# Kernel tuning notes

Hardware: AMD Instinct MI355X
Metric: run time of the kernel (lower is better)

The kernel has to match this reference:

```python
import jax, jax.numpy as jnp
import numpy as np

DIM = 512
DIM_TIME = 64
DIM_FF = 2048
B, L = 2, 512
EPS = 1e-5


def _layer_norm(x, g, b):
    mu = jnp.mean(x, axis=-1, keepdims=True)
    var = jnp.mean((x - mu) ** 2, axis=-1, keepdims=True)
    return (x - mu) * jax.lax.rsqrt(var + EPS) * g + b


def _sioconv(u, wa, hid_re, hid_im):
    # u: (B, L, Dt) float. Faithful to the FFT/triu construction, expressed as
    # cumulative log-sums (linear conv with all-ones == causal cumsum).
    Bb, Ll, Dt = u.shape
    out = (u @ wa.T).reshape(Bb, Ll, Dt, 2)          # linear_a, view_as_complex
    a_sqr = out[..., 0] ** 2 + out[..., 1] ** 2
    a = (out[..., 0] + 1j * out[..., 1]) * (jax.lax.rsqrt(a_sqr) * jnp.exp(-a_sqr))
    a = jnp.transpose(a, (0, 2, 1))                  # (B, Dt, L)
    a_ln = jnp.log(a)
    S = jnp.cumsum(a_ln, axis=-1)                    # S_k = sum_{j<=k} ln a_j
    S_prev = jnp.concatenate([jnp.zeros_like(S[..., :1]), S[..., :-1]], axis=-1)
    # c[b,d,i,k] = exp(S_k - S_{i-1}) = prod_{j=i..k} a_j, kept for k >= i-1
    diff = S[:, :, None, :] - S_prev[:, :, :, None]  # (B, Dt, L, L)
    idx = jnp.arange(Ll)
    mask = idx[None, :] >= (idx[:, None] - 1)        # k >= i-1 (triu diag=-1)
    c = jnp.where(mask, jnp.exp(diff), 0.0)
    uc = jnp.transpose(u.astype(jnp.complex64), (0, 2, 1))   # (B, Dt, L)
    hidden = (hid_re + 1j * hid_im)[None, :] * jnp.ones((Bb, 1), jnp.complex64)
    xin = jnp.concatenate([hidden[..., None], uc[..., :-1]], axis=-1)  # rolled + h0
    h = jnp.einsum('bdik,bdk->bdi', c, xin)
    h = h.at[:, :, -1].add(uc[:, :, -1])
    return jnp.transpose(h.real, (0, 2, 1)).astype(u.dtype)


def _ffn(x, w1, b1, w2, b2):
    return jax.nn.silu(x @ w1.T + b1) @ w2.T + b2


def setup_inputs() -> dict:
    key = jax.random.key(0)
    ks = jax.random.split(key, 12)
    d, dt, dff = DIM, DIM_TIME, DIM_FF
    return {
        'x': jax.random.normal(ks[0], (B, L, d), jnp.float32),
        'ln1_g': jnp.ones((d,), jnp.float32), 'ln1_b': jnp.zeros((d,), jnp.float32),
        'fc_w': jax.random.normal(ks[1], (dt, d), jnp.float32) * d ** -0.5,
        'fc_b': jnp.zeros((dt,), jnp.float32),
        'lin_in_w': jax.random.normal(ks[2], (dt, d), jnp.float32) * d ** -0.5,
        'lin_in_b': jnp.zeros((dt,), jnp.float32),
        'wa': jax.random.normal(ks[3], (2 * dt, dt), jnp.float32) * dt ** -0.5,
        'hid_re': jax.random.normal(ks[4], (dt,), jnp.float32),
        'hid_im': jax.random.normal(ks[5], (dt,), jnp.float32),
        'lin_out_w': jax.random.normal(ks[6], (d, dt), jnp.float32) * dt ** -0.5,
        'lin_out_b': jnp.zeros((d,), jnp.float32),
        'ln2_g': jnp.ones((d,), jnp.float32), 'ln2_b': jnp.zeros((d,), jnp.float32),
        'w1': jax.random.normal(ks[7], (dff, d), jnp.float32) * d ** -0.5,
        'b1': jnp.zeros((dff,), jnp.float32),
        'w2': jax.random.normal(ks[8], (d, dff), jnp.float32) * dff ** -0.5,
        'b2': jnp.zeros((d,), jnp.float32),
    }


def reference(x, ln1_g, ln1_b, fc_w, fc_b, lin_in_w, lin_in_b, wa, hid_re, hid_im,
              lin_out_w, lin_out_b, ln2_g, ln2_b, w1, b1, w2, b2):
    x_res = x
    xn = _layer_norm(x, ln1_g, ln1_b)
    y = jax.nn.silu(xn @ fc_w.T + fc_b)                  # gate, (B, L, Dt)
    u = xn @ lin_in_w.T + lin_in_b                       # (B, L, Dt)
    h = _sioconv(u, wa, hid_re, hid_im)
    x = (h * y) @ lin_out_w.T + lin_out_b + x_res        # dropout = identity (eval)
    x_res = x
    x = _ffn(_layer_norm(x, ln2_g, ln2_b), w1, b1, w2, b2) + x_res
    return x
```

## Files before the change

### kernel.cpp

```cpp
#include <hip/hip_runtime.h>
#include <math.h>

#define LSEQ 512
#define DMODEL 512
#define DT 64
#define DFF 2048

typedef unsigned short u16;
typedef __attribute__((ext_vector_type(8))) short short8;
typedef __attribute__((ext_vector_type(4))) float f32x4;
typedef __attribute__((ext_vector_type(16))) float f32x16;

__device__ __forceinline__ float wave_sum(float v) {
#pragma unroll
  for (int o = 32; o > 0; o >>= 1) v += __shfl_xor(v, o, 64);
  return v;
}

__device__ __forceinline__ u16 f2bf(float f) {
  unsigned int u = __float_as_uint(f);
  u += 0x7fffu + ((u >> 16) & 1u);
  return (u16)(u >> 16);
}
__device__ __forceinline__ float bf2f(u16 h) {
  return __uint_as_float(((unsigned int)h) << 16);
}
__device__ __forceinline__ void splitbf(float f, u16& h, u16& l) {
  h = f2bf(f);
  l = f2bf(f - bf2f(h));
}
__device__ __forceinline__ void split8(const float* __restrict__ p,
                                       short8& bh, short8& bl) {
  float4 a = *(const float4*)p;
  float4 b = *(const float4*)(p + 4);
  float vv[8] = {a.x, a.y, a.z, a.w, b.x, b.y, b.z, b.w};
#pragma unroll
  for (int e = 0; e < 8; ++e) {
    u16 h, l; splitbf(vv[e], h, l);
    bh[e] = (short)h; bl[e] = (short)l;
  }
}


__global__ __launch_bounds__(512) void k_fa(
    const float* __restrict__ x, const float* __restrict__ g1,
    const float* __restrict__ be1,
    const float* __restrict__ fcw, const float* __restrict__ liw,
    const float* __restrict__ wa,
    const float* __restrict__ fcb, const float* __restrict__ lib,
    const float* __restrict__ w1, const float* __restrict__ w2,
    float* __restrict__ y_o, float* __restrict__ u_o,
    float* __restrict__ ar_o, float* __restrict__ ai_o,
    u16* __restrict__ w1s, u16* __restrict__ w2s)
{
  const int blk = blockIdx.x;
  if (blk >= 64) {
    for (int i = (blk - 64) * 512 + threadIdx.x; i < 524288; i += 131072) {
      if (i < 262144) {
        int r = i >> 7, c0 = (i & 127) << 2;
        float4 v = ((const float4*)w1)[i];
        ushort4 o;
        o.x = f2bf(v.x); o.y = f2bf(v.y); o.z = f2bf(v.z); o.w = f2bf(v.w);
        int lane_s = (r & 31) + (((c0 & 15) >> 3) << 5);
        int flat = (r >> 5) * 16384 + (c0 >> 4) * 512 + lane_s * 8 + (c0 & 7);
        *(ushort4*)(w1s + flat) = o;
      } else {
        int ii = i - 262144;
        int r = ii >> 9, c0 = (ii & 511) << 2;
        float4 v = ((const float4*)w2)[ii];
        ushort4 o;
        o.x = f2bf(v.x); o.y = f2bf(v.y); o.z = f2bf(v.z); o.w = f2bf(v.w);
        int lane_s = (r & 31) + (((c0 & 15) >> 3) << 5);
        int flat = (r >> 5) * 65536 + (c0 >> 4) * 512 + lane_s * 8 + (c0 & 7);
        *(ushort4*)(w2s + flat) = o;
      }
    }
    return;
  }
  __shared__ __align__(16) u16 xsh[16][520];
  __shared__ __align__(16) u16 xsl[16][520];
  __shared__ __align__(16) u16 ush[16][80];
  __shared__ __align__(16) u16 usl[16][80];
  const int tid = threadIdx.x;
  const int wv = tid >> 6, lane = tid & 63;
  const int lr = lane & 15, lk = lane >> 4;
  const int mt = blk;

#pragma unroll
  for (int rr = 0; rr < 2; ++rr) {
    const int r = wv * 2 + rr;
    const int row = mt * 16 + r;
    const float* xr = x + (size_t)row * DMODEL;
    float v[8]; float s = 0.f;
#pragma unroll
    for (int j = 0; j < 8; ++j) { v[j] = xr[lane + 64 * j]; s += v[j]; }
    s = wave_sum(s);
    const float mu = s * (1.f / 512.f);
    float q = 0.f;
#pragma unroll
    for (int j = 0; j < 8; ++j) { float dd = v[j] - mu; q += dd * dd; }
    q = wave_sum(q);
    const float rstd = rsqrtf(q * (1.f / 512.f) + 1e-5f);
#pragma unroll
    for (int j = 0; j < 8; ++j) {
      int idx = lane + 64 * j;
      float o = (v[j] - mu) * rstd * g1[idx] + be1[idx];
      u16 h, l; splitbf(o, h, l);
      xsh[r][idx] = h;
      xsl[r][idx] = l;
    }
  }
  __syncthreads();

  const int c = wv * 16 + lr;
  {
    const float* brow = (c < DT) ? (fcw + (size_t)c * DMODEL)
                                 : (liw + (size_t)(c - DT) * DMODEL);
    f32x4 acc = {};
#pragma unroll 4
    for (int k = 0; k < DMODEL; k += 32) {
      short8 ah = *(const short8*)&xsh[lr][k + lk * 8];
      short8 al = *(const short8*)&xsl[lr][k + lk * 8];
      short8 bh, bl;
      split8(brow + k + lk * 8, bh, bl);
      acc = __builtin_amdgcn_mfma_f32_16x16x32_bf16(ah, bh, acc, 0, 0, 0);
      acc = __builtin_amdgcn_mfma_f32_16x16x32_bf16(ah, bl, acc, 0, 0, 0);
      acc = __builtin_amdgcn_mfma_f32_16x16x32_bf16(al, bh, acc, 0, 0, 0);
    }
#pragma unroll
    for (int j = 0; j < 4; ++j) {
      int rl = lk * 4 + j;
      int row = mt * 16 + rl;
      float v = acc[j];
      if (c < DT) {
        v += fcb[c];
        y_o[row * DT + c] = v / (1.f + expf(-v));
      } else {
        int d = c - DT;
        v += lib[d];
        u_o[row * DT + d] = v;
        u16 h, l; splitbf(v, h, l);
        ush[rl][d] = h; usl[rl][d] = l;
      }
    }
  }
  __syncthreads();
  {
    const float* warow = wa + (size_t)c * DT;
    f32x4 acc = {};
#pragma unroll
    for (int ks = 0; ks < 2; ++ks) {
      short8 ah = *(const short8*)&ush[lr][ks * 32 + lk * 8];
      short8 al = *(const short8*)&usl[lr][ks * 32 + lk * 8];
      short8 bh, bl;
      split8(warow + ks * 32 + lk * 8, bh, bl);
      acc = __builtin_amdgcn_mfma_f32_16x16x32_bf16(ah, bh, acc, 0, 0, 0);
      acc = __builtin_amdgcn_mfma_f32_16x16x32_bf16(ah, bl, acc, 0, 0, 0);
      acc = __builtin_amdgcn_mfma_f32_16x16x32_bf16(al, bh, acc, 0, 0, 0);
    }
#pragma unroll
    for (int j = 0; j < 4; ++j) {
      float v = acc[j];
      float p = __shfl_xor(v, 1, 64);
      float re = (lane & 1) ? p : v;
      float im = (lane & 1) ? v : p;
      float asq = re * re + im * im;
      float sc = rsqrtf(asq) * expf(-asq);
      int row = mt * 16 + lk * 4 + j;
      int d = c >> 1;
      if (lane & 1) ai_o[row * DT + d] = im * sc;
      else          ar_o[row * DT + d] = re * sc;
    }
  }
}

__global__ __launch_bounds__(64) void k_scan2(
    const float* __restrict__ u, const float* __restrict__ ar, const float* __restrict__ ai,
    const float* __restrict__ hr, const float* __restrict__ hi, float* __restrict__ h_o)
{
  const int blk = blockIdx.x;
  const int b = blk >> 6, d = blk & 63;
  const int lane = threadIdx.x;
  const size_t base = (size_t)b * LSEQ * DT + d;
  const int i0 = lane * 8;

  float a_r[8], a_i[8], b_r[8], b_i[8];
#pragma unroll
  for (int e = 0; e < 8; ++e) {
    int i = i0 + e;
    a_r[e] = ar[base + (size_t)i * DT];
    a_i[e] = ai[base + (size_t)i * DT];
    if (i >= 2)      { b_r[e] = u[base + (size_t)(i - 2) * DT]; b_i[e] = 0.f; }
    else if (i == 1) { b_r[e] = hr[d]; b_i[e] = hi[d]; }
    else             { b_r[e] = 0.f;   b_i[e] = 0.f; }
  }

  float Ar = 1.f, Ai = 0.f, Br = 0.f, Bi = 0.f;
#pragma unroll
  for (int e = 0; e < 8; ++e) {
    float nBr = fmaf(Ar, b_r[e], fmaf(-Ai, b_i[e], Br));
    float nBi = fmaf(Ar, b_i[e], fmaf( Ai, b_r[e], Bi));
    float nAr = Ar * a_r[e] - Ai * a_i[e];
    float nAi = Ar * a_i[e] + Ai * a_r[e];
    Ar = nAr; Ai = nAi; Br = nBr; Bi = nBi;
  }

#pragma unroll
  for (int dlt = 1; dlt < 64; dlt <<= 1) {
    float Ar2 = __shfl_down(Ar, dlt, 64);
    float Ai2 = __shfl_down(Ai, dlt, 64);
    float Br2 = __shfl_down(Br, dlt, 64);
    float Bi2 = __shfl_down(Bi, dlt, 64);
    if (lane + dlt < 64) {
      float nAr = Ar * Ar2 - Ai * Ai2;
      float nAi = Ar * Ai2 + Ai * Ar2;
      float nBr = fmaf(Ar, Br2, fmaf(-Ai, Bi2, Br));
      float nBi = fmaf(Ar, Bi2, fmaf( Ai, Br2, Bi));
      Ar = nAr; Ai = nAi; Br = nBr; Bi = nBi;
    }
  }

  float A1r = __shfl_down(Ar, 1, 64), A1i = __shfl_down(Ai, 1, 64);
  float B1r = __shfl_down(Br, 1, 64), B1i = __shfl_down(Bi, 1, 64);
  if (lane == 63) { A1r = 1.f; A1i = 0.f; B1r = 0.f; B1i = 0.f; }
  const float r512 = u[base + (size_t)(LSEQ - 2) * DT];
  float rr = fmaf(A1r, r512, B1r);
  float ri = fmaf(A1i, r512, B1i);

  const float uL = u[base + (size_t)(LSEQ - 1) * DT];
#pragma unroll
  for (int e = 7; e >= 0; --e) {
    int i = i0 + e;
    float nr = fmaf(a_r[e], rr, fmaf(-a_i[e], ri, b_r[e]));
    float ni = fmaf(a_r[e], ri, fmaf( a_i[e], rr, b_i[e]));
    rr = nr; ri = ni;
    float outv = rr;
    if (i == LSEQ - 1) outv += uL;
    h_o[base + (size_t)i * DT] = outv;
  }
}

__global__ __launch_bounds__(1024) void k_midln(
    const float* __restrict__ h, const float* __restrict__ y,
    const float* __restrict__ low, const float* __restrict__ lob,
    const float* __restrict__ x, const float* __restrict__ g2,
    const float* __restrict__ be2,
    float* __restrict__ x2_o, u16* __restrict__ xn2s)
{
  __shared__ __align__(16) u16 hyh[16][80];
  __shared__ __align__(16) u16 hyl[16][80];
  __shared__ float x2s[16][520];
  const int tid = threadIdx.x;
  const int w = tid >> 6, lane = tid & 63;
  const int lr = lane & 15, lk = lane >> 4;
  const int mt = blockIdx.x;

  {
    int r = tid >> 6, d = tid & 63;
    int row = mt * 16 + r;
    float v = h[row * DT + d] * y[row * DT + d];
    u16 hh, ll; splitbf(v, hh, ll);
    hyh[r][d] = hh; hyl[r][d] = ll;
  }
  __syncthreads();

#pragma unroll
  for (int t = 0; t < 2; ++t) {
    const int nt = w * 2 + t;
    const float* brow = low + (size_t)(nt * 16 + lr) * DT;
    f32x4 acc = {};
#pragma unroll
    for (int ks = 0; ks < 2; ++ks) {
      short8 ah = *(const short8*)&hyh[lr][ks * 32 + lk * 8];
      short8 al = *(const short8*)&hyl[lr][ks * 32 + lk * 8];
      short8 bh, bl;
      split8(brow + ks * 32 + lk * 8, bh, bl);
      acc = __builtin_amdgcn_mfma_f32_16x16x32_bf16(ah, bh, acc, 0, 0, 0);
      acc = __builtin_amdgcn_mfma_f32_16x16x32_bf16(ah, bl, acc, 0, 0, 0);
      acc = __builtin_amdgcn_mfma_f32_16x16x32_bf16(al, bh, acc, 0, 0, 0);
    }
    const int c = nt * 16 + lr;
#pragma unroll
    for (int j = 0; j < 4; ++j) {
      int rl = lk * 4 + j;
      int row = mt * 16 + rl;
      float v = acc[j] + lob[c] + x[(size_t)row * DMODEL + c];
      x2s[rl][c] = v;
      x2_o[(size_t)row * DMODEL + c] = v;
    }
  }
  __syncthreads();

  {
    const int r = w;
    const int row = mt * 16 + r;
    float v[8]; float s = 0.f;
#pragma unroll
    for (int j = 0; j < 8; ++j) { v[j] = x2s[r][lane + 64 * j]; s += v[j]; }
    s = wave_sum(s);
    const float mu = s * (1.f / 512.f);
    float q = 0.f;
#pragma unroll
    for (int j = 0; j < 8; ++j) { float dd = v[j] - mu; q += dd * dd; }
    q = wave_sum(q);
    const float rstd = rsqrtf(q * (1.f / 512.f) + 1e-5f);
    const int t32 = row >> 5, r32 = row & 31;
#pragma unroll
    for (int j = 0; j < 8; ++j) {
      int idx = lane + 64 * j;
      float o = (v[j] - mu) * rstd * g2[idx] + be2[idx];
      int lane_s = r32 + (((idx & 15) >> 3) << 5);
      xn2s[t32 * 16384 + (idx >> 4) * 512 + lane_s * 8 + (idx & 7)] = f2bf(o);
    }
  }
}

__global__ __launch_bounds__(256) void k_ffn1(
    const u16* __restrict__ As, const u16* __restrict__ Bs,
    const float* __restrict__ bias, u16* __restrict__ Cs)
{
  const int w = threadIdx.x >> 6, lane = threadIdx.x & 63;
  const int mt = blockIdx.x, nt = blockIdx.y * 4 + w;
  const u16* a = As + mt * 16384 + lane * 8;
  const u16* b = Bs + nt * 16384 + lane * 8;
  f32x16 acc = {};
#pragma unroll 8
  for (int kb = 0; kb < 32; ++kb)
    acc = __builtin_amdgcn_mfma_f32_32x32x16_bf16(*(const short8*)(a + kb * 512),
                                                  *(const short8*)(b + kb * 512),
                                                  acc, 0, 0, 0);
  const int l31 = lane & 31, hi = lane >> 5;
  const int col = nt * 32 + l31;
  const float bb = bias[col];
  const int kb_c = col >> 4;
  const int half_c = (col & 15) >> 3, e_c = col & 7;
#pragma unroll
  for (int r = 0; r < 16; ++r) {
    int row32 = (r & 3) + 8 * (r >> 2) + 4 * hi;
    float v = acc[r] + bb;
    v = v / (1.f + expf(-v));
    int lane_s = row32 + (half_c << 5);
    Cs[mt * 65536 + kb_c * 512 + lane_s * 8 + e_c] = f2bf(v);
  }
}

__global__ __launch_bounds__(256) void k_ffn2(
    const u16* __restrict__ As, const u16* __restrict__ Bs,
    const float* __restrict__ b2, const float* __restrict__ x2,
    float* __restrict__ out)
{
  __shared__ float red[4][16][64];
  const int w = threadIdx.x >> 6, lane = threadIdx.x & 63;
  const int mt = blockIdx.x, nt = blockIdx.y;
  const u16* a = As + mt * 65536 + w * 32 * 512 + lane * 8;
  const u16* b = Bs + nt * 65536 + w * 32 * 512 + lane * 8;
  f32x16 acc = {};
#pragma unroll 8
  for (int kb = 0; kb < 32; ++kb)
    acc = __builtin_amdgcn_mfma_f32_32x32x16_bf16(*(const short8*)(a + kb * 512),
                                                  *(const short8*)(b + kb * 512),
                                                  acc, 0, 0, 0);
#pragma unroll
  for (int r = 0; r < 16; ++r) red[w][r][lane] = acc[r];
  __syncthreads();
  for (int s = threadIdx.x; s < 1024; s += 256) {
    int r = s >> 6, l = s & 63;
    float v = red[0][r][l] + red[1][r][l] + red[2][r][l] + red[3][r][l];
    int row = mt * 32 + (r & 3) + 8 * (r >> 2) + 4 * (l >> 5);
    int col = nt * 32 + (l & 31);
    out[(size_t)row * DMODEL + col] =
        v + b2[col] + x2[(size_t)row * DMODEL + col];
  }
}

extern "C" void kernel_launch(void* const* d_in, const int* in_sizes, int n_in,
                              void* d_out, int out_size, void* d_ws, size_t ws_size,
                              hipStream_t stream) {
  const float* x    = (const float*)d_in[0];
  const float* ln1g = (const float*)d_in[1];
  const float* ln1b = (const float*)d_in[2];
  const float* fcw  = (const float*)d_in[3];
  const float* fcb  = (const float*)d_in[4];
  const float* liw  = (const float*)d_in[5];
  const float* lib  = (const float*)d_in[6];
  const float* wa   = (const float*)d_in[7];
  const float* hidr = (const float*)d_in[8];
  const float* hidi = (const float*)d_in[9];
  const float* low  = (const float*)d_in[10];
  const float* lob  = (const float*)d_in[11];
  const float* ln2g = (const float*)d_in[12];
  const float* ln2b = (const float*)d_in[13];
  const float* w1   = (const float*)d_in[14];
  const float* b1   = (const float*)d_in[15];
  const float* w2   = (const float*)d_in[16];
  const float* b2   = (const float*)d_in[17];
  float* out = (float*)d_out;
  float* ws  = (float*)d_ws;

  float* y_   = ws;
  float* u_   = y_  + 65536;
  float* ar_  = u_  + 65536;
  float* ai_  = ar_ + 65536;
  float* h_   = ai_ + 65536;
  float* x2_  = h_  + 65536;
  u16* p = (u16*)(x2_ + 524288);
  u16* xn2s = p;            p += 524288;
  u16* h1s  = p;            p += 2097152;
  u16* w1s  = p;            p += 1048576;
  u16* w2s  = p;            p += 1048576;

  k_fa<<<320, 512, 0, stream>>>(x, ln1g, ln1b, fcw, liw, wa, fcb, lib, w1, w2,
                                y_, u_, ar_, ai_, w1s, w2s);
  k_scan2<<<128, 64, 0, stream>>>(u_, ar_, ai_, hidr, hidi, h_);
  k_midln<<<64, 1024, 0, stream>>>(h_, y_, low, lob, x, ln2g, ln2b, x2_, xn2s);
  k_ffn1<<<dim3(32, 16), 256, 0, stream>>>(xn2s, w1s, b1, h1s);
  k_ffn2<<<dim3(32, 16), 256, 0, stream>>>(h1s, w2s, b2, x2_, out);
}
```

Baseline: 53.72 us.

## Fuse mid LayerNorm and both FFN GEMMs into one per-row-tile kernel

Merges the residual/LayerNorm kernel and the two FFN GEMM kernels into a single k_tail kernel with 64 blocks of 1024 threads. Each block keeps its 16 rows of x2 and normalized activations in shared memory and runs both GEMMs with 16x16x32 MFMAs. Weights are repacked into 16-row tiles to match. This removes two launches and the x2/xn2 round trips through global memory. In exchange the FFN runs on only 64 blocks, and every block streams the full W1 and W2 from cache, so parallelism drops sharply and weight traffic grows.

```diff
diff --git a/kernel.cpp b/kernel.cpp
--- a/kernel.cpp
+++ b/kernel.cpp
@@ -9,7 +9,6 @@
 typedef unsigned short u16;
 typedef __attribute__((ext_vector_type(8))) short short8;
 typedef __attribute__((ext_vector_type(4))) float f32x4;
-typedef __attribute__((ext_vector_type(16))) float f32x16;
 
 __device__ __forceinline__ float wave_sum(float v) {
 #pragma unroll
@@ -61,8 +60,8 @@
         float4 v = ((const float4*)w1)[i];
         ushort4 o;
         o.x = f2bf(v.x); o.y = f2bf(v.y); o.z = f2bf(v.z); o.w = f2bf(v.w);
-        int lane_s = (r & 31) + (((c0 & 15) >> 3) << 5);
-        int flat = (r >> 5) * 16384 + (c0 >> 4) * 512 + lane_s * 8 + (c0 & 7);
+        int flat = (r >> 4) * 8192 + (c0 >> 5) * 512 +
+                   ((r & 15) + 16 * ((c0 & 31) >> 3)) * 8 + (c0 & 7);
         *(ushort4*)(w1s + flat) = o;
       } else {
         int ii = i - 262144;
@@ -70,8 +69,8 @@
         float4 v = ((const float4*)w2)[ii];
         ushort4 o;
         o.x = f2bf(v.x); o.y = f2bf(v.y); o.z = f2bf(v.z); o.w = f2bf(v.w);
-        int lane_s = (r & 31) + (((c0 & 15) >> 3) << 5);
-        int flat = (r >> 5) * 65536 + (c0 >> 4) * 512 + lane_s * 8 + (c0 & 7);
+        int flat = (r >> 4) * 32768 + (c0 >> 5) * 512 +
+                   ((r & 15) + 16 * ((c0 & 31) >> 3)) * 8 + (c0 & 7);
         *(ushort4*)(w2s + flat) = o;
       }
     }
@@ -240,18 +239,21 @@
   }
 }
 
-__global__ __launch_bounds__(1024) void k_midln(
+__global__ __launch_bounds__(1024) void k_tail(
     const float* __restrict__ h, const float* __restrict__ y,
     const float* __restrict__ low, const float* __restrict__ lob,
     const float* __restrict__ x, const float* __restrict__ g2,
     const float* __restrict__ be2,
-    float* __restrict__ x2_o, u16* __restrict__ xn2s)
+    const float* __restrict__ b1, const float* __restrict__ b2,
+    const u16* __restrict__ w1s, const u16* __restrict__ w2s,
+    u16* __restrict__ h1s, float* __restrict__ out)
 {
   __shared__ __align__(16) u16 hyh[16][80];
   __shared__ __align__(16) u16 hyl[16][80];
   __shared__ float x2s[16][520];
+  __shared__ __align__(16) u16 xn2[16][520];
   const int tid = threadIdx.x;
-  const int w = tid >> 6, lane = tid & 63;
+  const int wv = tid >> 6, lane = tid & 63;
   const int lr = lane & 15, lk = lane >> 4;
   const int mt = blockIdx.x;
 
@@ -266,7 +268,7 @@
 
 #pragma unroll
   for (int t = 0; t < 2; ++t) {
-    const int nt = w * 2 + t;
+    const int nt = wv * 2 + t;
     const float* brow = low + (size_t)(nt * 16 + lr) * DT;
     f32x4 acc = {};
 #pragma unroll
@@ -284,16 +286,13 @@
     for (int j = 0; j < 4; ++j) {
       int rl = lk * 4 + j;
       int row = mt * 16 + rl;
-      float v = acc[j] + lob[c] + x[(size_t)row * DMODEL + c];
-      x2s[rl][c] = v;
-      x2_o[(size_t)row * DMODEL + c] = v;
-    }
-  }
-  __syncthreads();
-
-  {
-    const int r = w;
-    const int row = mt * 16 + r;
+      x2s[rl][c] = acc[j] + lob[c] + x[(size_t)row * DMODEL + c];
+    }
+  }
+  __syncthreads();
+
+  {
+    const int r = wv;
     float v[8]; float s = 0.f;
 #pragma unroll
     for (int j = 0; j < 8; ++j) { v[j] = x2s[r][lane + 64 * j]; s += v[j]; }
@@ -304,72 +303,61 @@
     for (int j = 0; j < 8; ++j) { float dd = v[j] - mu; q += dd * dd; }
     q = wave_sum(q);
     const float rstd = rsqrtf(q * (1.f / 512.f) + 1e-5f);
-    const int t32 = row >> 5, r32 = row & 31;
 #pragma unroll
     for (int j = 0; j < 8; ++j) {
       int idx = lane + 64 * j;
-      float o = (v[j] - mu) * rstd * g2[idx] + be2[idx];
-      int lane_s = r32 + (((idx & 15) >> 3) << 5);
-      xn2s[t32 * 16384 + (idx >> 4) * 512 + lane_s * 8 + (idx & 7)] = f2bf(o);
-    }
-  }
-}
-
-__global__ __launch_bounds__(256) void k_ffn1(
-    const u16* __restrict__ As, const u16* __restrict__ Bs,
-    const float* __restrict__ bias, u16* __restrict__ Cs)
-{
-  const int w = threadIdx.x >> 6, lane = threadIdx.x & 63;
-  const int mt = blockIdx.x, nt = blockIdx.y * 4 + w;
-  const u16* a = As + mt * 16384 + lane * 8;
-  const u16* b = Bs + nt * 16384 + lane * 8;
-  f32x16 acc = {};
-#pragma unroll 8
-  for (int kb = 0; kb < 32; ++kb)
-    acc = __builtin_amdgcn_mfma_f32_32x32x16_bf16(*(const short8*)(a + kb * 512),
-                                                  *(const short8*)(b + kb * 512),
-                                                  acc, 0, 0, 0);
-  const int l31 = lane & 31, hi = lane >> 5;
-  const int col = nt * 32 + l31;
-  const float bb = bias[col];
-  const int kb_c = col >> 4;
-  const int half_c = (col & 15) >> 3, e_c = col & 7;
-#pragma unroll
-  for (int r = 0; r < 16; ++r) {
-    int row32 = (r & 3) + 8 * (r >> 2) + 4 * hi;
-    float v = acc[r] + bb;
-    v = v / (1.f + expf(-v));
-    int lane_s = row32 + (half_c << 5);
-    Cs[mt * 65536 + kb_c * 512 + lane_s * 8 + e_c] = f2bf(v);
-  }
-}
-
-__global__ __launch_bounds__(256) void k_ffn2(
-    const u16* __restrict__ As, const u16* __restrict__ Bs,
-    const float* __restrict__ b2, const float* __restrict__ x2,
-    float* __restrict__ out)
-{
-  __shared__ float red[4][16][64];
-  const int w = threadIdx.x >> 6, lane = threadIdx.x & 63;
-  const int mt = blockIdx.x, nt = blockIdx.y;
-  const u16* a = As + mt * 65536 + w * 32 * 512 + lane * 8;
-  const u16* b = Bs + nt * 65536 + w * 32 * 512 + lane * 8;
-  f32x16 acc = {};
-#pragma unroll 8
-  for (int kb = 0; kb < 32; ++kb)
-    acc = __builtin_amdgcn_mfma_f32_32x32x16_bf16(*(const short8*)(a + kb * 512),
-                                                  *(const short8*)(b + kb * 512),
-                                                  acc, 0, 0, 0);
-#pragma unroll
-  for (int r = 0; r < 16; ++r) red[w][r][lane] = acc[r];
-  __syncthreads();
-  for (int s = threadIdx.x; s < 1024; s += 256) {
-    int r = s >> 6, l = s & 63;
-    float v = red[0][r][l] + red[1][r][l] + red[2][r][l] + red[3][r][l];
-    int row = mt * 32 + (r & 3) + 8 * (r >> 2) + 4 * (l >> 5);
-    int col = nt * 32 + (l & 31);
-    out[(size_t)row * DMODEL + col] =
-        v + b2[col] + x2[(size_t)row * DMODEL + col];
+      xn2[r][idx] = f2bf((v[j] - mu) * rstd * g2[idx] + be2[idx]);
+    }
+  }
+  __syncthreads();
+
+  {
+#pragma unroll
+    for (int tt = 0; tt < 8; ++tt) {
+      const int t = wv * 8 + tt;
+      const u16* b = w1s + t * 8192 + lane * 8;
+      f32x4 acc = {};
+#pragma unroll
+      for (int kb = 0; kb < 16; ++kb) {
+        short8 af = *(const short8*)&xn2[lr][kb * 32 + lk * 8];
+        short8 bf = *(const short8*)(b + kb * 512);
+        acc = __builtin_amdgcn_mfma_f32_16x16x32_bf16(af, bf, acc, 0, 0, 0);
+      }
+      const int col = t * 16 + lr;
+      const float bb = b1[col];
+      const int kb2 = col >> 5, hi2 = (col & 31) >> 3, e2 = col & 7;
+#pragma unroll
+      for (int j = 0; j < 4; ++j) {
+        int row16 = lk * 4 + j;
+        float v = acc[j] + bb;
+        v = v / (1.f + expf(-v));
+        h1s[mt * 32768 + kb2 * 512 + (row16 + 16 * hi2) * 8 + e2] = f2bf(v);
+      }
+    }
+  }
+  __syncthreads();
+
+  {
+#pragma unroll
+    for (int tt = 0; tt < 2; ++tt) {
+      const int t2 = wv * 2 + tt;
+      const u16* a = h1s + mt * 32768 + lane * 8;
+      const u16* b = w2s + t2 * 32768 + lane * 8;
+      f32x4 acc = {};
+      for (int kb = 0; kb < 64; ++kb) {
+        short8 af = *(const short8*)(a + kb * 512);
+        short8 bf = *(const short8*)(b + kb * 512);
+        acc = __builtin_amdgcn_mfma_f32_16x16x32_bf16(af, bf, acc, 0, 0, 0);
+      }
+      const int col = t2 * 16 + lr;
+      const float bb = b2[col];
+#pragma unroll
+      for (int j = 0; j < 4; ++j) {
+        int row16 = lk * 4 + j;
+        int row = mt * 16 + row16;
+        out[(size_t)row * DMODEL + col] = acc[j] + bb + x2s[row16][col];
+      }
+    }
   }
 }
 
@@ -402,9 +390,7 @@
   float* ar_  = u_  + 65536;
   float* ai_  = ar_ + 65536;
   float* h_   = ai_ + 65536;
-  float* x2_  = h_  + 65536;
-  u16* p = (u16*)(x2_ + 524288);
-  u16* xn2s = p;            p += 524288;
+  u16* p = (u16*)(h_ + 65536);
   u16* h1s  = p;            p += 2097152;
   u16* w1s  = p;            p += 1048576;
   u16* w2s  = p;            p += 1048576;
@@ -412,7 +398,6 @@
   k_fa<<<320, 512, 0, stream>>>(x, ln1g, ln1b, fcw, liw, wa, fcb, lib, w1, w2,
                                 y_, u_, ar_, ai_, w1s, w2s);
   k_scan2<<<128, 64, 0, stream>>>(u_, ar_, ai_, hidr, hidi, h_);
-  k_midln<<<64, 1024, 0, stream>>>(h_, y_, low, lob, x, ln2g, ln2b, x2_, xn2s);
-  k_ffn1<<<dim3(32, 16), 256, 0, stream>>>(xn2s, w1s, b1, h1s);
-  k_ffn2<<<dim3(32, 16), 256, 0, stream>>>(h1s, w2s, b2, x2_, out);
-}
+  k_tail<<<64, 1024, 0, stream>>>(h_, y_, low, lob, x, ln2g, ln2b, b1, b2,
+                                  w1s, w2s, h1s, out);
+}
```

Measured after the change: 91.07 us. 1.7x slower.

## Fuse mid layernorm with FFN first GEMM into one kernel

Applied to the files above, without the earlier changes.

Merges the post-conv projection plus residual plus LayerNorm kernel with the FFN up-projection kernel. Each 16-row tile is now handled by four blocks, and each block recomputes the small lin_out GEMM and the LayerNorm before doing one quarter of the W1 columns with 16x16x32 MFMAs. The W1 pre-swizzle layout is changed to match. This removes one kernel launch and the global round trip of the normalized activations. In exchange the cheap front part is computed four times and the 32x32 MFMA tiles are replaced by smaller ones.

```diff
diff --git a/kernel.cpp b/kernel.cpp
--- a/kernel.cpp
+++ b/kernel.cpp
@@ -61,8 +61,8 @@
         float4 v = ((const float4*)w1)[i];
         ushort4 o;
         o.x = f2bf(v.x); o.y = f2bf(v.y); o.z = f2bf(v.z); o.w = f2bf(v.w);
-        int lane_s = (r & 31) + (((c0 & 15) >> 3) << 5);
-        int flat = (r >> 5) * 16384 + (c0 >> 4) * 512 + lane_s * 8 + (c0 & 7);
+        int flat = (r >> 4) * 8192 + (c0 >> 5) * 512 +
+                   ((r & 15) + 16 * ((c0 & 31) >> 3)) * 8 + (c0 & 7);
         *(ushort4*)(w1s + flat) = o;
       } else {
         int ii = i - 262144;
@@ -240,23 +240,27 @@
   }
 }
 
-__global__ __launch_bounds__(1024) void k_midln(
+__global__ __launch_bounds__(512) void k_mfl(
     const float* __restrict__ h, const float* __restrict__ y,
     const float* __restrict__ low, const float* __restrict__ lob,
     const float* __restrict__ x, const float* __restrict__ g2,
-    const float* __restrict__ be2,
-    float* __restrict__ x2_o, u16* __restrict__ xn2s)
+    const float* __restrict__ be2, const float* __restrict__ b1,
+    const u16* __restrict__ w1s,
+    float* __restrict__ x2_o, u16* __restrict__ h1s)
 {
   __shared__ __align__(16) u16 hyh[16][80];
   __shared__ __align__(16) u16 hyl[16][80];
   __shared__ float x2s[16][520];
+  __shared__ __align__(16) u16 xn2[16][520];
   const int tid = threadIdx.x;
-  const int w = tid >> 6, lane = tid & 63;
+  const int wv = tid >> 6, lane = tid & 63;
   const int lr = lane & 15, lk = lane >> 4;
-  const int mt = blockIdx.x;
-
-  {
-    int r = tid >> 6, d = tid & 63;
+  const int mt = blockIdx.x >> 2, chunk = blockIdx.x & 3;
+
+#pragma unroll
+  for (int it = 0; it < 2; ++it) {
+    int idx = it * 512 + tid;
+    int r = idx >> 6, d = idx & 63;
     int row = mt * 16 + r;
     float v = h[row * DT + d] * y[row * DT + d];
     u16 hh, ll; splitbf(v, hh, ll);
@@ -265,8 +269,8 @@
   __syncthreads();
 
 #pragma unroll
-  for (int t = 0; t < 2; ++t) {
-    const int nt = w * 2 + t;
+  for (int t = 0; t < 4; ++t) {
+    const int nt = wv * 4 + t;
     const float* brow = low + (size_t)(nt * 16 + lr) * DT;
     f32x4 acc = {};
 #pragma unroll
@@ -286,14 +290,14 @@
       int row = mt * 16 + rl;
       float v = acc[j] + lob[c] + x[(size_t)row * DMODEL + c];
       x2s[rl][c] = v;
-      x2_o[(size_t)row * DMODEL + c] = v;
-    }
-  }
-  __syncthreads();
-
-  {
-    const int r = w;
-    const int row = mt * 16 + r;
+      if (chunk == 0) x2_o[(size_t)row * DMODEL + c] = v;
+    }
+  }
+  __syncthreads();
+
+#pragma unroll
+  for (int rr = 0; rr < 2; ++rr) {
+    const int r = wv * 2 + rr;
     float v[8]; float s = 0.f;
 #pragma unroll
     for (int j = 0; j < 8; ++j) { v[j] = x2s[r][lane + 64 * j]; s += v[j]; }
@@ -304,43 +308,39 @@
     for (int j = 0; j < 8; ++j) { float dd = v[j] - mu; q += dd * dd; }
     q = wave_sum(q);
     const float rstd = rsqrtf(q * (1.f / 512.f) + 1e-5f);
-    const int t32 = row >> 5, r32 = row & 31;
 #pragma unroll
     for (int j = 0; j < 8; ++j) {
       int idx = lane + 64 * j;
-      float o = (v[j] - mu) * rstd * g2[idx] + be2[idx];
-      int lane_s = r32 + (((idx & 15) >> 3) << 5);
-      xn2s[t32 * 16384 + (idx >> 4) * 512 + lane_s * 8 + (idx & 7)] = f2bf(o);
-    }
-  }
-}
-
-__global__ __launch_bounds__(256) void k_ffn1(
-    const u16* __restrict__ As, const u16* __restrict__ Bs,
-    const float* __restrict__ bias, u16* __restrict__ Cs)
-{
-  const int w = threadIdx.x >> 6, lane = threadIdx.x & 63;
-  const int mt = blockIdx.x, nt = blockIdx.y * 4 + w;
-  const u16* a = As + mt * 16384 + lane * 8;
-  const u16* b = Bs + nt * 16384 + lane * 8;
-  f32x16 acc = {};
-#pragma unroll 8
-  for (int kb = 0; kb < 32; ++kb)
-    acc = __builtin_amdgcn_mfma_f32_32x32x16_bf16(*(const short8*)(a + kb * 512),
-                                                  *(const short8*)(b + kb * 512),
-                                                  acc, 0, 0, 0);
-  const int l31 = lane & 31, hi = lane >> 5;
-  const int col = nt * 32 + l31;
-  const float bb = bias[col];
-  const int kb_c = col >> 4;
-  const int half_c = (col & 15) >> 3, e_c = col & 7;
-#pragma unroll
-  for (int r = 0; r < 16; ++r) {
-    int row32 = (r & 3) + 8 * (r >> 2) + 4 * hi;
-    float v = acc[r] + bb;
-    v = v / (1.f + expf(-v));
-    int lane_s = row32 + (half_c << 5);
-    Cs[mt * 65536 + kb_c * 512 + lane_s * 8 + e_c] = f2bf(v);
+      xn2[r][idx] = f2bf((v[j] - mu) * rstd * g2[idx] + be2[idx]);
+    }
+  }
+  __syncthreads();
+
+  {
+    const int t32 = mt >> 1;
+#pragma unroll
+    for (int tt = 0; tt < 4; ++tt) {
+      const int t = chunk * 32 + wv * 4 + tt;
+      const u16* b = w1s + t * 8192 + lane * 8;
+      f32x4 acc = {};
+#pragma unroll
+      for (int kb = 0; kb < 16; ++kb) {
+        short8 af = *(const short8*)&xn2[lr][kb * 32 + lk * 8];
+        short8 bf = *(const short8*)(b + kb * 512);
+        acc = __builtin_amdgcn_mfma_f32_16x16x32_bf16(af, bf, acc, 0, 0, 0);
+      }
+      const int col = t * 16 + lr;
+      const float bb = b1[col];
+#pragma unroll
+      for (int j = 0; j < 4; ++j) {
+        int row16 = lk * 4 + j;
+        float v = acc[j] + bb;
+        v = v / (1.f + expf(-v));
+        int r32 = (mt & 1) * 16 + row16;
+        int lane_s = r32 + 32 * (lr >> 3);
+        h1s[t32 * 65536 + t * 512 + lane_s * 8 + (lr & 7)] = f2bf(v);
+      }
+    }
   }
 }
 
@@ -404,7 +404,6 @@
   float* h_   = ai_ + 65536;
   float* x2_  = h_  + 65536;
   u16* p = (u16*)(x2_ + 524288);
-  u16* xn2s = p;            p += 524288;
   u16* h1s  = p;            p += 2097152;
   u16* w1s  = p;            p += 1048576;
   u16* w2s  = p;            p += 1048576;
@@ -412,7 +411,7 @@
   k_fa<<<320, 512, 0, stream>>>(x, ln1g, ln1b, fcw, liw, wa, fcb, lib, w1, w2,
                                 y_, u_, ar_, ai_, w1s, w2s);
   k_scan2<<<128, 64, 0, stream>>>(u_, ar_, ai_, hidr, hidi, h_);
-  k_midln<<<64, 1024, 0, stream>>>(h_, y_, low, lob, x, ln2g, ln2b, x2_, xn2s);
-  k_ffn1<<<dim3(32, 16), 256, 0, stream>>>(xn2s, w1s, b1, h1s);
+  k_mfl<<<256, 512, 0, stream>>>(h_, y_, low, lob, x, ln2g, ln2b, b1,
+                                 w1s, x2_, h1s);
   k_ffn2<<<dim3(32, 16), 256, 0, stream>>>(h1s, w2s, b2, x2_, out);
 }
```

Result: no change. 53.41 us (median of 2 runs) (-0.6%).
